# Kernel optimization log

Hardware: AMD Instinct MI355X
Metric: run time of the kernel (lower is better)

Reference implementation:

```python
import jax, jax.numpy as jnp
import numpy as np

B, T, M, D, V = 4, 256, 512, 1024, 50257


def setup_inputs() -> dict:
    key = jax.random.key(0)
    ks = jax.random.split(key, 10)
    s = 0.02  # weight init scale
    return {
        "decoder_output": jax.random.normal(ks[0], (B, T, D), jnp.float32),
        "memory_output": jax.random.normal(ks[1], (B, M, D), jnp.float32),
        "memory_sequence_length": jax.random.randint(ks[2], (B,), 1, M + 1),
        "memory_ids": jax.random.randint(ks[3], (B, M), 0, V),
        "W_copy": jax.random.normal(ks[4], (D, D), jnp.float32) * s,
        "b_copy": jnp.zeros((D,), jnp.float32),
        "W_dec": jax.random.normal(ks[5], (D, 2 * D), jnp.float32) * s,
        "b_dec": jnp.zeros((D,), jnp.float32),
        "W_gen": jax.random.normal(ks[6], (1, D), jnp.float32) * s,
        "b_gen": jnp.zeros((1,), jnp.float32),
        "W_out": jax.random.normal(ks[7], (V, D), jnp.float32) * s,
        "b_out": jnp.zeros((V,), jnp.float32),
    }


def reference(decoder_output, memory_output, memory_sequence_length, memory_ids,
              W_copy, b_copy, W_dec, b_dec, W_gen, b_gen, W_out, b_out):
    # apply_copy_attn (standard mechanism)
    mem_proj = jnp.einsum('bmd,ed->bme', memory_output, W_copy) + b_copy     # [B,M,D]
    scores = jnp.einsum('btd,bmd->btm', decoder_output, mem_proj)            # [B,T,M]
    mask = jnp.arange(M) < memory_sequence_length[:, None]                   # [B,M]
    scores = jnp.where(mask[:, None, :], scores, -jnp.inf)
    attn_scores = jax.nn.softmax(scores, axis=-1)                            # [B,T,M]
    attn_output = jnp.einsum('btm,bmd->btd', attn_scores, memory_output)     # [B,T,D]

    # compute_logits_with_copy_attn
    dec_cat = jnp.concatenate([decoder_output, attn_output], axis=-1)        # [B,T,2D]
    dec_with_attn = jnp.tanh(jnp.einsum('bte,de->btd', dec_cat, W_dec) + b_dec)
    orig_logits = jnp.einsum('btd,vd->btv', decoder_output, W_out) + b_out   # [B,T,V]
    p_gen = jax.nn.sigmoid(jnp.einsum('btd,od->bto', dec_with_attn, W_gen) + b_gen)  # [B,T,1]
    gen_probs = jax.nn.softmax(orig_logits, axis=-1) * p_gen                 # [B,T,V]
    copy_probs = attn_scores * (1.0 - p_gen)                                 # [B,T,M]

    # scatter_add copy probs into the vocab distribution
    b_idx = jnp.arange(B)[:, None, None]
    t_idx = jnp.arange(T)[None, :, None]
    v_idx = memory_ids[:, None, :]                                           # [B,1,M]
    final = gen_probs.at[b_idx, t_idx, v_idx].add(copy_probs)
    return jnp.log(final)
```

## Files before the change

### kernel.cpp

```cpp
#include <hip/hip_runtime.h>
#include <math.h>

#define DIV_UP(a,b) (((a)+(b)-1)/(b))

static constexpr int Bb = 4, Tt = 256, Mm = 512, Dd = 1024, Vv = 50257;
static constexpr int NN = Bb * Tt;

typedef __attribute__((ext_vector_type(8))) short short8v;
typedef __attribute__((ext_vector_type(4))) float float4v;
typedef unsigned short ushort;

static __device__ __forceinline__ ushort f2bf(float f) {
    unsigned u = __float_as_uint(f);
    u += 0x7FFFu + ((u >> 16) & 1u);
    return (ushort)(u >> 16);
}
static __device__ __forceinline__ float bf2f(ushort h) {
    return __uint_as_float(((unsigned)h) << 16);
}

static __device__ __forceinline__ void gload16(const void* g, void* l) {
    __builtin_amdgcn_global_load_lds(
        (const __attribute__((address_space(1))) unsigned int*)g,
        (__attribute__((address_space(3))) unsigned int*)l, 16, 0, 0);
}

static constexpr long PN0 = (long)NN * Dd / 8;
static constexpr long PN1 = (long)Bb * Mm * Dd / 8;
static constexpr long PN2 = (long)Dd * 2 * Dd / 8;
static constexpr long PN3 = (long)Vv * Dd / 8;
static constexpr long PTOT = PN0 + PN1 + PN2 + PN3;

__launch_bounds__(256)
__global__ void prep_all(const float* __restrict__ dec, ushort* __restrict__ A16,
                         ushort* __restrict__ dec_lo,
                         const float* __restrict__ mem, ushort* __restrict__ mem_hi,
                         ushort* __restrict__ mem_lo,
                         const float* __restrict__ Wd, ushort* __restrict__ Wd16,
                         const float* __restrict__ Wo, ushort* __restrict__ B16)
{
    for (long i = blockIdx.x * 256 + threadIdx.x; i < PTOT; i += (long)gridDim.x * 256) {
        const float* src; ushort* hi; ushort* lo = nullptr; long off;
        if (i < PN0)                  { src = dec; hi = A16;    lo = dec_lo; off = i; }
        else if (i < PN0 + PN1)       { src = mem; hi = mem_hi; lo = mem_lo; off = i - PN0; }
        else if (i < PN0 + PN1 + PN2) { src = Wd;  hi = Wd16;   off = i - PN0 - PN1; }
        else                          { src = Wo;  hi = B16;    off = i - PN0 - PN1 - PN2; }

        const float4 v0 = *(const float4*)&src[off * 8];
        const float4 v1 = *(const float4*)&src[off * 8 + 4];
        short8v th, tl;
#pragma unroll
        for (int q = 0; q < 4; ++q) {
            float a = (q < 1 ? v0.x : q < 2 ? v0.y : q < 3 ? v0.z : v0.w);
            (void)a;
        }
        float vs[8] = {v0.x, v0.y, v0.z, v0.w, v1.x, v1.y, v1.z, v1.w};
#pragma unroll
        for (int q = 0; q < 8; ++q) {
            ushort h = f2bf(vs[q]);
            th[q] = h;
            tl[q] = f2bf(vs[q] - bf2f(h));
        }
        *(short8v*)&hi[off * 8] = th;
        if (lo) *(short8v*)&lo[off * 8] = tl;
    }
}

__launch_bounds__(256)
__global__ void transpose_split(const float* __restrict__ in, ushort* __restrict__ oh,
                                ushort* __restrict__ ol, int R, int C)
{
    __shared__ float t[32][33];
    const int bz = blockIdx.z;
    in += (long)bz * R * C;
    oh += (long)bz * R * C;
    if (ol) ol += (long)bz * R * C;
    const int tx = threadIdx.x & 31, ty = threadIdx.x >> 5;
    const int r0 = blockIdx.y * 32, c0 = blockIdx.x * 32;
#pragma unroll
    for (int k = 0; k < 4; ++k)
        t[ty + k * 8][tx] = in[(long)(r0 + ty + k * 8) * C + c0 + tx];
    __syncthreads();
#pragma unroll
    for (int k = 0; k < 4; ++k) {
        float v = t[tx][ty + k * 8];
        ushort h = f2bf(v);
        long o = (long)(c0 + ty + k * 8) * R + r0 + tx;
        oh[o] = h;
        if (ol) ol[o] = f2bf(v - bf2f(h));
    }
}

template<bool SPLIT, int MREP>
__launch_bounds__(256)
__global__ void gemm_mx(const ushort* __restrict__ Ah, const ushort* __restrict__ Al,
                        const ushort* __restrict__ Bh, const ushort* __restrict__ Bl,
                        const ushort* __restrict__ A2, int ksplit, int lda2,
                        const float* __restrict__ bias,
                        float* __restrict__ Cf, ushort* __restrict__ C16,
                        float* __restrict__ aux, const float* __restrict__ Wg,
                        int Ncols, int K, int lda, int ldb, int ldc,
                        long sA, long sB, long sC, int epi)
{
    constexpr int BM    = MREP * 32;
    constexpr int ATILE = BM * 32;
    constexpr int BTILE = 4096;
    constexpr int BUF   = (SPLIT ? 2 : 1) * (ATILE + BTILE);
    __shared__ __align__(16) ushort lds[2 * BUF];

    const int jt = blockIdx.x, mt = blockIdx.y, bz = blockIdx.z;

    const int tid  = threadIdx.x;
    const int lane = tid & 63;
    const int wave = tid >> 6;
    const int mw = (wave >> 1) * (MREP * 16), nw = (wave & 1) * 64;
    const int i0 = mt * BM, j0 = jt * 128;

    const int srow = tid >> 2;
    const int soff = ((tid & 3) ^ ((srow >> 1) & 3)) * 8;

    const long Ab = (long)bz * sA;
    const long Bz = (long)bz * sB;
    const long ar0 = i0 + srow, ar1 = i0 + 64 + srow;
    long br0 = j0 + srow;      if (br0 > Ncols - 1) br0 = Ncols - 1;
    long br1 = j0 + 64 + srow; if (br1 > Ncols - 1) br1 = Ncols - 1;

    const int NT = K >> 5;
    const int fr = lane & 15;
    const int rdsw = ((lane >> 4) ^ ((fr >> 1) & 3)) * 8;

    float4v acc[MREP][4];
#pragma unroll
    for (int m = 0; m < MREP; ++m)
#pragma unroll
        for (int n = 0; n < 4; ++n) acc[m][n] = (float4v){0.f, 0.f, 0.f, 0.f};

    auto STAGE = [&](int buf, int kc) {
        ushort* base = lds + buf * BUF;
        if constexpr (SPLIT) {
            const ushort* pAh = Ah + Ab; const ushort* pAl = Al + Ab;
            const ushort* pBh = Bh + Bz; const ushort* pBl = Bl + Bz;
            gload16(&pAh[ar0 * lda + kc + soff], base + tid * 8);
            if constexpr (MREP == 4)
                gload16(&pAh[ar1 * lda + kc + soff], base + 2048 + tid * 8);
            ushort* bAl = base + ATILE;
            gload16(&pAl[ar0 * lda + kc + soff], bAl + tid * 8);
            if constexpr (MREP == 4)
                gload16(&pAl[ar1 * lda + kc + soff], bAl + 2048 + tid * 8);
            ushort* bBh = base + 2 * ATILE;
            gload16(&pBh[br0 * ldb + kc + soff], bBh + tid * 8);
            gload16(&pBh[br1 * ldb + kc + soff], bBh + 2048 + tid * 8);
            ushort* bBl = bBh + BTILE;
            gload16(&pBl[br0 * ldb + kc + soff], bBl + tid * 8);
            gload16(&pBl[br1 * ldb + kc + soff], bBl + 2048 + tid * 8);
        } else {
            const bool sec = kc >= ksplit;
            const int  kk  = sec ? kc - ksplit : kc;
            const int  lA  = sec ? lda2 : lda;
            const ushort* Asrc = (sec ? A2 : Ah) + Ab;
            gload16(&Asrc[ar0 * (long)lA + kk + soff], base + tid * 8);
            if constexpr (MREP == 4)
                gload16(&Asrc[ar1 * (long)lA + kk + soff], base + 2048 + tid * 8);
            ushort* bB = base + ATILE;
            const ushort* pB = Bh + Bz;
            gload16(&pB[br0 * ldb + kc + soff], bB + tid * 8);
            gload16(&pB[br1 * ldb + kc + soff], bB + 2048 + tid * 8);
        }
    };

    STAGE(0, 0);
    __syncthreads();
    for (int t = 0; t < NT; ++t) {
        const int cur = t & 1;
        const ushort* Acur = lds + cur * BUF;
        const ushort* Bcur = Acur + (SPLIT ? 2 * ATILE : ATILE);

        if (t + 1 < NT) STAGE(cur ^ 1, (t + 1) * 32);

        short8v a[MREP], b[4];
#pragma unroll
        for (int m = 0; m < MREP; ++m)
            a[m] = *(const short8v*)&Acur[(mw + m * 16 + fr) * 32 + rdsw];
#pragma unroll
        for (int n = 0; n < 4; ++n)
            b[n] = *(const short8v*)&Bcur[(nw + n * 16 + fr) * 32 + rdsw];

        if constexpr (SPLIT) {
            short8v al[MREP], bl[4];
#pragma unroll
            for (int m = 0; m < MREP; ++m)
                al[m] = *(const short8v*)&Acur[ATILE + (mw + m * 16 + fr) * 32 + rdsw];
#pragma unroll
            for (int n = 0; n < 4; ++n)
                bl[n] = *(const short8v*)&Bcur[BTILE + (nw + n * 16 + fr) * 32 + rdsw];
#pragma unroll
            for (int m = 0; m < MREP; ++m)
#pragma unroll
                for (int n = 0; n < 4; ++n) {
                    acc[m][n] = __builtin_amdgcn_mfma_f32_16x16x32_bf16(a[m],  b[n],  acc[m][n], 0, 0, 0);
                    acc[m][n] = __builtin_amdgcn_mfma_f32_16x16x32_bf16(a[m],  bl[n], acc[m][n], 0, 0, 0);
                    acc[m][n] = __builtin_amdgcn_mfma_f32_16x16x32_bf16(al[m], b[n],  acc[m][n], 0, 0, 0);
                }
        } else {
#pragma unroll
            for (int m = 0; m < MREP; ++m)
#pragma unroll
                for (int n = 0; n < 4; ++n)
                    acc[m][n] = __builtin_amdgcn_mfma_f32_16x16x32_bf16(a[m], b[n], acc[m][n], 0, 0, 0);
        }
        __syncthreads();
    }

    const int fc = lane & 15;
    const int fq = (lane >> 4) * 4;

    float red[4][4];
#pragma unroll
    for (int m = 0; m < 4; ++m)
#pragma unroll
        for (int q = 0; q < 4; ++q) red[m][q] = 0.f;

    ushort* lo16 = (ushort*)aux;

#pragma unroll
    for (int n = 0; n < 4; ++n) {
        const int col = j0 + nw + n * 16 + fc;
        if (col >= Ncols) continue;
        const float bc = bias ? bias[col] : 0.f;
        const float wg = (epi == 2) ? Wg[col] : 0.f;
#pragma unroll
        for (int m = 0; m < MREP; ++m) {
            const int r0 = i0 + mw + m * 16 + fq;
            float4v v = acc[m][n];
#pragma unroll
            for (int q = 0; q < 4; ++q) {
                float x = v[q] + bc;
                const long ci = (long)bz * sC + (long)(r0 + q) * ldc + col;
                if (epi == 0) {
                    Cf[ci] = x;
                } else if (epi == 2) {
                    red[m][q] += tanhf(x) * wg;
                } else if (epi == 3) {
                    ushort h = f2bf(x);
                    C16[ci] = h;
                    lo16[ci] = f2bf(x - bf2f(h));
                } else {
                    C16[ci] = f2bf(x);
                }
            }
        }
    }
    if (epi == 2) {
#pragma unroll
        for (int m = 0; m < MREP; ++m)
#pragma unroll
            for (int q = 0; q < 4; ++q) {
                float s = red[m][q];
                s += __shfl_xor(s, 1);
                s += __shfl_xor(s, 2);
                s += __shfl_xor(s, 4);
                s += __shfl_xor(s, 8);
                if (fc == 0)
                    atomicAdd(&aux[i0 + mw + m * 16 + fq + q], s);
            }
    }
}

__launch_bounds__(256, 4)
__global__ void gemm_logits(const ushort* __restrict__ A,
                            const ushort* __restrict__ B,
                            const float* __restrict__ bias,
                            float* __restrict__ C,
                            float* __restrict__ rowsum,
                            int Ncols, int K, int xcd_jtiles)
{
    constexpr int TILE = 4096;
    __shared__ __align__(16) ushort lds[4 * TILE];

    const int id = blockIdx.x;
    const int s = id >> 3;
    const int jt = (id & 7) * ((xcd_jtiles + 7) >> 3) + (s >> 3);
    const int mt = s & 7;
    if (jt >= xcd_jtiles) return;

    const int tid  = threadIdx.x;
    const int lane = tid & 63;
    const int wave = tid >> 6;
    const int mw = (wave >> 1) * 64, nw = (wave & 1) * 64;
    const int i0 = mt * 128, j0 = jt * 128;

    const int srow = tid >> 2;
    const int soff = ((tid & 3) ^ ((srow >> 1) & 3)) * 8;

    const long ar0 = i0 + srow, ar1 = i0 + 64 + srow;
    long br0 = j0 + srow;      if (br0 > Ncols - 1) br0 = Ncols - 1;
    long br1 = j0 + 64 + srow; if (br1 > Ncols - 1) br1 = Ncols - 1;

    const int NT = K >> 5;
    const int fr = lane & 15;
    const int rdsw = ((lane >> 4) ^ ((fr >> 1) & 3)) * 8;

    float4v acc[4][4];
#pragma unroll
    for (int m = 0; m < 4; ++m)
#pragma unroll
        for (int n = 0; n < 4; ++n) acc[m][n] = (float4v){0.f, 0.f, 0.f, 0.f};

    auto STAGE = [&](int buf, int kc) {
        ushort* base = lds + buf * 2 * TILE;
        gload16(&A[ar0 * K + kc + soff], base + tid * 8);
        gload16(&A[ar1 * K + kc + soff], base + 2048 + tid * 8);
        ushort* bB = base + TILE;
        gload16(&B[br0 * K + kc + soff], bB + tid * 8);
        gload16(&B[br1 * K + kc + soff], bB + 2048 + tid * 8);
    };

    STAGE(0, 0);
    __syncthreads();
    for (int t = 0; t < NT; ++t) {
        const int cur = t & 1;
        const ushort* Acur = lds + cur * 2 * TILE;
        const ushort* Bcur = Acur + TILE;

        if (t + 1 < NT) STAGE(cur ^ 1, (t + 1) * 32);

        short8v a[4], b[4];
#pragma unroll
        for (int m = 0; m < 4; ++m)
            a[m] = *(const short8v*)&Acur[(mw + m * 16 + fr) * 32 + rdsw];
#pragma unroll
        for (int n = 0; n < 4; ++n)
            b[n] = *(const short8v*)&Bcur[(nw + n * 16 + fr) * 32 + rdsw];

#pragma unroll
        for (int m = 0; m < 4; ++m)
#pragma unroll
            for (int n = 0; n < 4; ++n)
                acc[m][n] = __builtin_amdgcn_mfma_f32_16x16x32_bf16(a[m], b[n], acc[m][n], 0, 0, 0);
        __syncthreads();
    }

    const int fc = lane & 15;
    const int fq = (lane >> 4) * 4;
    constexpr int TS = 132;
    float* T = (float*)lds;
    const int r  = tid >> 3;
    const int cg = tid & 7;
    const int csw = (r & 3) << 2;
#pragma unroll
    for (int c = 0; c < 4; ++c) {
        __syncthreads();
        if ((wave >> 1) == (c >> 1)) {
#pragma unroll
            for (int mm = 0; mm < 2; ++mm) {
                const int m = (c & 1) * 2 + mm;
                const int lr = mm * 16 + fq;
#pragma unroll
                for (int n = 0; n < 4; ++n) {
                    float4v v = acc[m][n];
#pragma unroll
                    for (int q = 0; q < 4; ++q)
                        T[(lr + q) * TS +
                          ((nw + n * 16 + fc) ^ (((lr + q) & 3) << 2))] = v[q];
                }
            }
        }
        __syncthreads();
        const int grow = i0 + 32 * c + r;
        float sm = 0.f;
        float* po = &C[(long)grow * Ncols + j0 + cg * 16];
#pragma unroll
        for (int w4 = 0; w4 < 4; ++w4) {
            const int col = cg * 16 + w4 * 4;
            const int gc = j0 + col;
            const float4 tv = *(const float4*)&T[r * TS + (col ^ csw)];
            float vv[4] = {tv.x, tv.y, tv.z, tv.w};
#pragma unroll
            for (int q2 = 0; q2 < 4; ++q2) {
                if (gc + q2 < Ncols) {
                    vv[q2] += bias[gc + q2];
                    sm += __expf(vv[q2]);
                }
            }
            if (gc + 3 < Ncols) {
                *(float4*)(po + w4 * 4) = make_float4(vv[0], vv[1], vv[2], vv[3]);
            } else {
#pragma unroll
                for (int q2 = 0; q2 < 4; ++q2)
                    if (gc + q2 < Ncols) po[w4 * 4 + q2] = vv[q2];
            }
        }
        sm += __shfl_xor(sm, 1);
        sm += __shfl_xor(sm, 2);
        sm += __shfl_xor(sm, 4);
        if (cg == 0) atomicAdd(&rowsum[grow], sm);
    }
}

__global__ void softmax_rows(float* __restrict__ s, ushort* __restrict__ s16,
                             const int* __restrict__ msl,
                             float* __restrict__ rowsum, float* __restrict__ pgacc)
{
    __shared__ float red[256];
    const int row = blockIdx.x;
    const int b   = row / Tt;
    const int len = msl[b];
    float* p = s + (long)row * Mm;
    ushort* p16 = s16 + (long)row * Mm;
    const int tid = threadIdx.x;

    if (tid == 0) { rowsum[row] = 0.f; pgacc[row] = 0.f; }

    float v[2], mx = -INFINITY;
#pragma unroll
    for (int q = 0; q < 2; ++q) {
        int m = tid + q * 256;
        v[q] = (m < len) ? p[m] : -INFINITY;
        mx = fmaxf(mx, v[q]);
    }
    red[tid] = mx; __syncthreads();
    for (int off = 128; off > 0; off >>= 1) {
        if (tid < off) red[tid] = fmaxf(red[tid], red[tid + off]);
        __syncthreads();
    }
    mx = red[0]; __syncthreads();

    float e[2], sm = 0.f;
#pragma unroll
    for (int q = 0; q < 2; ++q) {
        int m = tid + q * 256;
        e[q] = (m < len) ? expf(v[q] - mx) : 0.f;
        sm += e[q];
    }
    red[tid] = sm; __syncthreads();
    for (int off = 128; off > 0; off >>= 1) {
        if (tid < off) red[tid] += red[tid + off];
        __syncthreads();
    }
    const float inv = 1.0f / red[0];
#pragma unroll
    for (int q = 0; q < 2; ++q) {
        float a = e[q] * inv;
        p[tid + q * 256] = a;
        p16[tid + q * 256] = f2bf(a);
    }
}

static constexpr int QS = 8;
static constexpr int QW = DIV_UP(Vv, QS);
__launch_bounds__(256)
__global__ void shift_rows(float* __restrict__ out, const float* __restrict__ pgacc,
                           const float* __restrict__ bg, const float* __restrict__ rowsum)
{
    const int row = blockIdx.y;
    const int qq  = blockIdx.x;
    const int tid = threadIdx.x;

    const int c0 = qq * QW;
    const int c1 = (c0 + QW < Vv) ? c0 + QW : Vv;
    const int cnt = c1 - c0;

    const float pgl = 1.0f / (1.0f + __expf(-(pgacc[row] + bg[0])));
    const float s = __logf(pgl / rowsum[row]);

    const long base = (long)row * Vv + c0;
    float* p = out + base;
    const int mis  = (int)(((unsigned)base) & 3u);
    int head = (4 - mis) & 3;
    if (head > cnt) head = cnt;
    if (tid < head) p[tid] += s;
    const int nv = (cnt - head) >> 2;
    float4* p4 = (float4*)(p + head);
    for (int i = tid; i < nv; i += 256) {
        float4 v = p4[i];
        v.x += s; v.y += s; v.z += s; v.w += s;
        p4[i] = v;
    }
    const int t = head + nv * 4 + tid;
    if (t < cnt) p[t] += s;
}

__launch_bounds__(256)
__global__ void fixup_rows(float* __restrict__ out, const float* __restrict__ attn,
                           const float* __restrict__ pgacc, const float* __restrict__ bg,
                           const int* __restrict__ ids, const int* __restrict__ msl)
{
    __shared__ int   hkey[1024];
    __shared__ float hval[1024];
    const int row = blockIdx.x;
    const int b   = row / Tt;
    const int len = msl[b];
    const int tid = threadIdx.x;

    const float pgl = 1.0f / (1.0f + __expf(-(pgacc[row] + bg[0])));
    const float c = 1.0f - pgl;

    for (int i = tid; i < 1024; i += 256) { hkey[i] = -1; hval[i] = 0.f; }
    __syncthreads();

    for (int m = tid; m < len; m += 256) {
        const int id = ids[(long)b * Mm + m];
        const float v = attn[(long)row * Mm + m] * c;
        unsigned h = ((unsigned)id * 2654435761u) >> 22;
        while (true) {
            int prev = atomicCAS(&hkey[h], -1, id);
            if (prev == -1 || prev == id) { atomicAdd(&hval[h], v); break; }
            h = (h + 1) & 1023u;
        }
    }
    __syncthreads();

    float* pr = out + (long)row * Vv;
    for (int i = tid; i < 1024; i += 256) {
        const int id = hkey[i];
        if (id >= 0) pr[id] = __logf(__expf(pr[id]) + hval[i]);
    }
}

extern "C" void kernel_launch(void* const* d_in, const int* in_sizes, int n_in,
                              void* d_out, int out_size, void* d_ws, size_t ws_size,
                              hipStream_t stream)
{
    const float* dec = (const float*)d_in[0];
    const float* mem = (const float*)d_in[1];
    const int*   msl = (const int*)d_in[2];
    const int*   ids = (const int*)d_in[3];
    const float* Wc  = (const float*)d_in[4];
    const float* Wd  = (const float*)d_in[6];
    const float* bd  = (const float*)d_in[7];
    const float* Wg  = (const float*)d_in[8];
    const float* bg  = (const float*)d_in[9];
    const float* Wo  = (const float*)d_in[10];
    const float* bo  = (const float*)d_in[11];

    float* out = (float*)d_out;

    float* ws     = (float*)d_ws;
    float* attn   = ws;
    float* rowsum = attn + (size_t)NN * Mm;
    float* pgacc  = rowsum + NN;
    ushort* A16   = (ushort*)(pgacc + NN);
    ushort* B16   = A16 + (size_t)NN * Dd;

    ushort* S      = (ushort*)d_out;
    ushort* dec_lo = S;
    ushort* WcT_hi = dec_lo + (size_t)NN * Dd;
    ushort* WcT_lo = WcT_hi + (size_t)Dd * Dd;
    ushort* mem_hi = WcT_lo + (size_t)Dd * Dd;
    ushort* mem_lo = mem_hi + (size_t)Bb * Mm * Dd;
    ushort* memT16 = mem_lo + (size_t)Bb * Mm * Dd;
    ushort* dp_hi  = memT16 + (size_t)Bb * Mm * Dd;
    ushort* dp_lo  = dp_hi + (size_t)NN * Dd;
    ushort* Wd16   = dp_lo + (size_t)NN * Dd;
    ushort* attn16 = Wd16 + (size_t)Dd * 2 * Dd;
    ushort* ao16   = attn16 + (size_t)NN * Mm;

    prep_all<<<4096, 256, 0, stream>>>(dec, A16, dec_lo, mem, mem_hi, mem_lo,
                                       Wd, Wd16, Wo, B16);
    transpose_split<<<dim3(Dd/32, Dd/32, 1), 256, 0, stream>>>(Wc, WcT_hi, WcT_lo, Dd, Dd);
    transpose_split<<<dim3(Dd/32, Mm/32, Bb), 256, 0, stream>>>(mem, memT16, nullptr, Mm, Dd);

    gemm_mx<true,2><<<dim3(Dd/128, NN/64, 1), 256, 0, stream>>>(
        A16, dec_lo, WcT_hi, WcT_lo, A16, Dd, Dd, nullptr,
        nullptr, dp_hi, (float*)dp_lo, nullptr,
        Dd, Dd, Dd, Dd, Dd, 0, 0, 0, 3);

    gemm_mx<true,2><<<dim3(Mm/128, Tt/64, Bb), 256, 0, stream>>>(
        dp_hi, dp_lo, mem_hi, mem_lo, dp_hi, Dd, Dd, nullptr,
        attn, nullptr, nullptr, nullptr,
        Mm, Dd, Dd, Dd, Mm, (long)Tt*Dd, (long)Mm*Dd, (long)Tt*Mm, 0);

    softmax_rows<<<NN, 256, 0, stream>>>(attn, attn16, msl, rowsum, pgacc);

    gemm_mx<false,2><<<dim3(Dd/128, Tt/64, Bb), 256, 0, stream>>>(
        attn16, attn16, memT16, memT16, attn16, Mm, Mm, nullptr,
        nullptr, ao16, nullptr, nullptr,
        Dd, Mm, Mm, Mm, Dd, (long)Tt*Mm, (long)Dd*Mm, (long)Tt*Dd, 4);

    gemm_mx<false,2><<<dim3(Dd/128, NN/64, 1), 256, 0, stream>>>(
        A16, A16, Wd16, Wd16, ao16, Dd, Dd, bd,
        nullptr, nullptr, pgacc, Wg,
        Dd, 2*Dd, Dd, 2*Dd, 0, 0, 0, 0, 2);

    gemm_logits<<<8 * 8 * DIV_UP(DIV_UP(Vv,128), 8), 256, 0, stream>>>(
        A16, B16, bo, out, rowsum, Vv, Dd, DIV_UP(Vv,128));

    shift_rows<<<dim3(QS, NN), 256, 0, stream>>>(out, pgacc, bg, rowsum);

    fixup_rows<<<NN, 256, 0, stream>>>(out, attn, pgacc, bg, ids, msl);
}
```

Baseline: 513.4 us.

## Shrink logits GEMM tile to 64x128 and write epilogue directly from registers

Changes the vocab-logits GEMM tile from 128x128 to 64x128, halving the A-tile LDS footprint and accumulator registers, and raises the occupancy hint to 5 blocks per CU. The LDS-transposed coalesced epilogue is replaced by direct per-lane scalar stores from MFMA accumulators with row-sum reduction via shuffles. This removes the epilogue syncs and LDS staging, but doubles B-matrix reloads (less reuse of W_out) and makes the output stores strided and less coalesced. A dead loop in the prep kernel is also removed.

After: 500.3 us, median of 2. -2.6%, faster.

```diff
diff --git a/kernel.cpp b/kernel.cpp
--- a/kernel.cpp
+++ b/kernel.cpp
@@ -49,11 +49,6 @@
         const float4 v0 = *(const float4*)&src[off * 8];
         const float4 v1 = *(const float4*)&src[off * 8 + 4];
         short8v th, tl;
-#pragma unroll
-        for (int q = 0; q < 4; ++q) {
-            float a = (q < 1 ? v0.x : q < 2 ? v0.y : q < 3 ? v0.z : v0.w);
-            (void)a;
-        }
         float vs[8] = {v0.x, v0.y, v0.z, v0.w, v1.x, v1.y, v1.z, v1.w};
 #pragma unroll
         for (int q = 0; q < 8; ++q) {
@@ -266,7 +261,7 @@
     }
 }
 
-__launch_bounds__(256, 4)
+__launch_bounds__(256, 5)
 __global__ void gemm_logits(const ushort* __restrict__ A,
                             const ushort* __restrict__ B,
                             const float* __restrict__ bias,
@@ -274,25 +269,27 @@
                             float* __restrict__ rowsum,
                             int Ncols, int K, int xcd_jtiles)
 {
-    constexpr int TILE = 4096;
-    __shared__ __align__(16) ushort lds[4 * TILE];
+    constexpr int ATILE = 2048;
+    constexpr int BTILE = 4096;
+    constexpr int BUF   = ATILE + BTILE;
+    __shared__ __align__(16) ushort lds[2 * BUF];
 
     const int id = blockIdx.x;
     const int s = id >> 3;
-    const int jt = (id & 7) * ((xcd_jtiles + 7) >> 3) + (s >> 3);
-    const int mt = s & 7;
+    const int jt = (id & 7) * ((xcd_jtiles + 7) >> 3) + (s >> 4);
+    const int mt = s & 15;
     if (jt >= xcd_jtiles) return;
 
     const int tid  = threadIdx.x;
     const int lane = tid & 63;
     const int wave = tid >> 6;
-    const int mw = (wave >> 1) * 64, nw = (wave & 1) * 64;
-    const int i0 = mt * 128, j0 = jt * 128;
+    const int mw = (wave >> 1) * 32, nw = (wave & 1) * 64;
+    const int i0 = mt * 64, j0 = jt * 128;
 
     const int srow = tid >> 2;
     const int soff = ((tid & 3) ^ ((srow >> 1) & 3)) * 8;
 
-    const long ar0 = i0 + srow, ar1 = i0 + 64 + srow;
+    const long ar0 = i0 + srow;
     long br0 = j0 + srow;      if (br0 > Ncols - 1) br0 = Ncols - 1;
     long br1 = j0 + 64 + srow; if (br1 > Ncols - 1) br1 = Ncols - 1;
 
@@ -300,17 +297,16 @@
     const int fr = lane & 15;
     const int rdsw = ((lane >> 4) ^ ((fr >> 1) & 3)) * 8;
 
-    float4v acc[4][4];
-#pragma unroll
-    for (int m = 0; m < 4; ++m)
+    float4v acc[2][4];
+#pragma unroll
+    for (int m = 0; m < 2; ++m)
 #pragma unroll
         for (int n = 0; n < 4; ++n) acc[m][n] = (float4v){0.f, 0.f, 0.f, 0.f};
 
     auto STAGE = [&](int buf, int kc) {
-        ushort* base = lds + buf * 2 * TILE;
+        ushort* base = lds + buf * BUF;
         gload16(&A[ar0 * K + kc + soff], base + tid * 8);
-        gload16(&A[ar1 * K + kc + soff], base + 2048 + tid * 8);
-        ushort* bB = base + TILE;
+        ushort* bB = base + ATILE;
         gload16(&B[br0 * K + kc + soff], bB + tid * 8);
         gload16(&B[br1 * K + kc + soff], bB + 2048 + tid * 8);
     };
@@ -319,21 +315,21 @@
     __syncthreads();
     for (int t = 0; t < NT; ++t) {
         const int cur = t & 1;
-        const ushort* Acur = lds + cur * 2 * TILE;
-        const ushort* Bcur = Acur + TILE;
+        const ushort* Acur = lds + cur * BUF;
+        const ushort* Bcur = Acur + ATILE;
 
         if (t + 1 < NT) STAGE(cur ^ 1, (t + 1) * 32);
 
-        short8v a[4], b[4];
-#pragma unroll
-        for (int m = 0; m < 4; ++m)
+        short8v a[2], b[4];
+#pragma unroll
+        for (int m = 0; m < 2; ++m)
             a[m] = *(const short8v*)&Acur[(mw + m * 16 + fr) * 32 + rdsw];
 #pragma unroll
         for (int n = 0; n < 4; ++n)
             b[n] = *(const short8v*)&Bcur[(nw + n * 16 + fr) * 32 + rdsw];
 
 #pragma unroll
-        for (int m = 0; m < 4; ++m)
+        for (int m = 0; m < 2; ++m)
 #pragma unroll
             for (int n = 0; n < 4; ++n)
                 acc[m][n] = __builtin_amdgcn_mfma_f32_16x16x32_bf16(a[m], b[n], acc[m][n], 0, 0, 0);
@@ -342,59 +338,42 @@
 
     const int fc = lane & 15;
     const int fq = (lane >> 4) * 4;
-    constexpr int TS = 132;
-    float* T = (float*)lds;
-    const int r  = tid >> 3;
-    const int cg = tid & 7;
-    const int csw = (r & 3) << 2;
-#pragma unroll
-    for (int c = 0; c < 4; ++c) {
-        __syncthreads();
-        if ((wave >> 1) == (c >> 1)) {
-#pragma unroll
-            for (int mm = 0; mm < 2; ++mm) {
-                const int m = (c & 1) * 2 + mm;
-                const int lr = mm * 16 + fq;
-#pragma unroll
-                for (int n = 0; n < 4; ++n) {
-                    float4v v = acc[m][n];
-#pragma unroll
-                    for (int q = 0; q < 4; ++q)
-                        T[(lr + q) * TS +
-                          ((nw + n * 16 + fc) ^ (((lr + q) & 3) << 2))] = v[q];
-                }
+
+    float red[2][4];
+#pragma unroll
+    for (int m = 0; m < 2; ++m)
+#pragma unroll
+        for (int q = 0; q < 4; ++q) red[m][q] = 0.f;
+
+#pragma unroll
+    for (int n = 0; n < 4; ++n) {
+        const int col = j0 + nw + n * 16 + fc;
+        if (col >= Ncols) continue;
+        const float bc = bias[col];
+#pragma unroll
+        for (int m = 0; m < 2; ++m) {
+            const int r0 = i0 + mw + m * 16 + fq;
+            float4v v = acc[m][n];
+#pragma unroll
+            for (int q = 0; q < 4; ++q) {
+                float x = v[q] + bc;
+                C[(long)(r0 + q) * Ncols + col] = x;
+                red[m][q] += __expf(x);
             }
         }
-        __syncthreads();
-        const int grow = i0 + 32 * c + r;
-        float sm = 0.f;
-        float* po = &C[(long)grow * Ncols + j0 + cg * 16];
-#pragma unroll
-        for (int w4 = 0; w4 < 4; ++w4) {
-            const int col = cg * 16 + w4 * 4;
-            const int gc = j0 + col;
-            const float4 tv = *(const float4*)&T[r * TS + (col ^ csw)];
-            float vv[4] = {tv.x, tv.y, tv.z, tv.w};
-#pragma unroll
-            for (int q2 = 0; q2 < 4; ++q2) {
-                if (gc + q2 < Ncols) {
-                    vv[q2] += bias[gc + q2];
-                    sm += __expf(vv[q2]);
-                }
-            }
-            if (gc + 3 < Ncols) {
-                *(float4*)(po + w4 * 4) = make_float4(vv[0], vv[1], vv[2], vv[3]);
-            } else {
-#pragma unroll
-                for (int q2 = 0; q2 < 4; ++q2)
-                    if (gc + q2 < Ncols) po[w4 * 4 + q2] = vv[q2];
-            }
-        }
-        sm += __shfl_xor(sm, 1);
-        sm += __shfl_xor(sm, 2);
-        sm += __shfl_xor(sm, 4);
-        if (cg == 0) atomicAdd(&rowsum[grow], sm);
-    }
+    }
+#pragma unroll
+    for (int m = 0; m < 2; ++m)
+#pragma unroll
+        for (int q = 0; q < 4; ++q) {
+            float sm = red[m][q];
+            sm += __shfl_xor(sm, 1);
+            sm += __shfl_xor(sm, 2);
+            sm += __shfl_xor(sm, 4);
+            sm += __shfl_xor(sm, 8);
+            if (fc == 0)
+                atomicAdd(&rowsum[i0 + mw + m * 16 + fq + q], sm);
+        }
 }
 
 __global__ void softmax_rows(float* __restrict__ s, ushort* __restrict__ s16,
@@ -582,7 +561,7 @@
         nullptr, nullptr, pgacc, Wg,
         Dd, 2*Dd, Dd, 2*Dd, 0, 0, 0, 0, 2);
 
-    gemm_logits<<<8 * 8 * DIV_UP(DIV_UP(Vv,128), 8), 256, 0, stream>>>(
+    gemm_logits<<<8 * 16 * DIV_UP(DIV_UP(Vv,128), 8), 256, 0, stream>>>(
         A16, B16, bo, out, rowsum, Vv, Dd, DIV_UP(Vv,128));
 
     shift_rows<<<dim3(QS, NN), 256, 0, stream>>>(out, pgacc, bg, rowsum);
```
